# Kernel optimization log

Measured on AMD Instinct MI355X. Metric: run time of the kernel, lower is better.

Reference implementation:

```python
import jax, jax.numpy as jnp
import numpy as np

IMG_C = 256
GC = 32  # graph_channel; must equal graph feature dim 32 for the residual


def setup_inputs() -> dict:
    key = jax.random.key(0)
    ks = jax.random.split(key, 10)
    B, N, WH_SIDE = 8, 4096, 64
    s = lambda fan_in: 1.0 / np.sqrt(fan_in)
    return {
        "input_graph": jax.random.normal(ks[0], (B, N, GC), jnp.float32),
        "input_image": jax.random.normal(ks[1], (B, IMG_C, WH_SIDE, WH_SIDE), jnp.float32),
        # Conv1d(kernel=1) weights stored as [out, in]
        "Wq": jax.random.uniform(ks[2], (GC, 32), jnp.float32, -s(32), s(32)),
        "bq": jax.random.uniform(ks[3], (GC,), jnp.float32, -s(32), s(32)),
        "Wk": jax.random.uniform(ks[4], (GC, IMG_C), jnp.float32, -s(IMG_C), s(IMG_C)),
        "bk": jax.random.uniform(ks[5], (GC,), jnp.float32, -s(IMG_C), s(IMG_C)),
        "Wv": jax.random.uniform(ks[6], (GC, IMG_C), jnp.float32, -s(IMG_C), s(IMG_C)),
        "bv": jax.random.uniform(ks[7], (GC,), jnp.float32, -s(IMG_C), s(IMG_C)),
        "Wc": jax.random.uniform(ks[8], (GC, GC), jnp.float32, -s(GC), s(GC)),
        "bc": jax.random.uniform(ks[9], (GC,), jnp.float32, -s(GC), s(GC)),
    }


def reference(input_graph, input_image, Wq, bq, Wk, bk, Wv, bv, Wc, bc):
    B, C, W, H = input_image.shape
    img = input_image.reshape(B, C, W * H)                      # [B, C, L]
    # 1x1 conv projections == channel matmuls
    K = jnp.einsum('oc,bcl->bol', Wk, img) + bk[None, :, None]  # [B, GC, L]
    V = jnp.einsum('oc,bcl->bol', Wv, img) + bv[None, :, None]  # [B, GC, L]
    # Q: graph [B, N, 32] -> conv over channel dim -> [B, N, GC]
    Q = jnp.einsum('oc,bnc->bno', Wq, input_graph) + bq[None, None, :]
    att = jnp.einsum('bno,bol->bnl', Q, K) / jnp.sqrt(jnp.float32(GC))  # [B, N, L]
    # NOTE: original softmax is over dim=1 (the node/query axis)
    att = jax.nn.softmax(att, axis=1)
    message = jnp.einsum('bol,bnl->bon', V, att)                # [B, GC, N]
    out = input_graph.transpose(0, 2, 1) + (
        jnp.einsum('oc,bcn->bon', Wc, message) + bc[None, :, None]
    )                                                           # [B, GC, N]
    return out.transpose(0, 2, 1)                               # [B, N, GC]
```

## Files before the change

### kernel.cpp

```cpp
#include <hip/hip_runtime.h>

#define BB 8
#define NN 4096
#define LL 4096
#define CC 256

typedef short bf16x8 __attribute__((ext_vector_type(8)));
typedef _Float16 f16x8 __attribute__((ext_vector_type(8)));
typedef __fp16 hf16x2 __attribute__((ext_vector_type(2)));
typedef float f32x4 __attribute__((ext_vector_type(4)));

__device__ __forceinline__ short f2bf(float f) {
  union { float f; unsigned u; } v; v.f = f;
  unsigned r = v.u + 0x7fffu + ((v.u >> 16) & 1u);
  return (short)(r >> 16);
}
__device__ __forceinline__ bf16x8 ld8(const float* __restrict__ fp) {
  float4 a = *(const float4*)fp;
  float4 b = *(const float4*)(fp + 4);
  bf16x8 r;
  r[0] = f2bf(a.x); r[1] = f2bf(a.y); r[2] = f2bf(a.z); r[3] = f2bf(a.w);
  r[4] = f2bf(b.x); r[5] = f2bf(b.y); r[6] = f2bf(b.z); r[7] = f2bf(b.w);
  return r;
}

__global__ __launch_bounds__(256) void ka_proj(
    const float* __restrict__ graph, const float* __restrict__ img,
    const float* __restrict__ Wq, const float* __restrict__ bq,
    const float* __restrict__ Wk, const float* __restrict__ bk,
    const float* __restrict__ Wv, const float* __restrict__ bv,
    short* __restrict__ Qb, short* __restrict__ Kt, _Float16* __restrict__ Vt,
    float* __restrict__ Zbuf)
{
  const int tid = threadIdx.x;
  const int w = tid >> 6, lane = tid & 63, lo = lane & 15, q = lane >> 4;
  const int bid = blockIdx.x;
  if (bid < 512) {
    const int b = bid >> 6;
    if (tid < 64) Zbuf[(size_t)b * LL + ((bid & 63) << 6) + tid] = 0.0f;
    const int lt = ((bid & 63) << 6) + (w << 4);
    f32x4 aK0 = {0,0,0,0}, aK1 = {0,0,0,0}, aV0 = {0,0,0,0}, aV1 = {0,0,0,0};
    const float* ib = img + (size_t)b * CC * LL + lt + lo;
    #pragma unroll
    for (int cs = 0; cs < 8; ++cs) {
      const int c0 = cs * 32 + q * 8;
      bf16x8 bi;
      #pragma unroll
      for (int j = 0; j < 8; ++j) bi[j] = f2bf(ib[(size_t)(c0 + j) * LL]);
      bf16x8 wk0 = ld8(Wk + lo * CC + c0);
      bf16x8 wk1 = ld8(Wk + (lo + 16) * CC + c0);
      bf16x8 wv0 = ld8(Wv + lo * CC + c0);
      bf16x8 wv1 = ld8(Wv + (lo + 16) * CC + c0);
      aK0 = __builtin_amdgcn_mfma_f32_16x16x32_bf16(wk0, bi, aK0, 0, 0, 0);
      aK1 = __builtin_amdgcn_mfma_f32_16x16x32_bf16(wk1, bi, aK1, 0, 0, 0);
      aV0 = __builtin_amdgcn_mfma_f32_16x16x32_bf16(wv0, bi, aV0, 0, 0, 0);
      aV1 = __builtin_amdgcn_mfma_f32_16x16x32_bf16(wv1, bi, aV1, 0, 0, 0);
    }
    const float kscale = 0.2550348663f;
    const size_t row = ((size_t)b * LL + lt + lo) * 32;
    short4 s0, s1;
    s0.x = f2bf((aK0[0] + bk[q * 4 + 0]) * kscale);
    s0.y = f2bf((aK0[1] + bk[q * 4 + 1]) * kscale);
    s0.z = f2bf((aK0[2] + bk[q * 4 + 2]) * kscale);
    s0.w = f2bf((aK0[3] + bk[q * 4 + 3]) * kscale);
    s1.x = f2bf((aK1[0] + bk[16 + q * 4 + 0]) * kscale);
    s1.y = f2bf((aK1[1] + bk[16 + q * 4 + 1]) * kscale);
    s1.z = f2bf((aK1[2] + bk[16 + q * 4 + 2]) * kscale);
    s1.w = f2bf((aK1[3] + bk[16 + q * 4 + 3]) * kscale);
    *(short4*)(Kt + row + q * 4) = s0;
    *(short4*)(Kt + row + 16 + q * 4) = s1;
    union { hf16x2 h[2]; uint2 u; } p0, p1;
    p0.h[0] = __builtin_amdgcn_cvt_pkrtz(aV0[0] + bv[q * 4 + 0], aV0[1] + bv[q * 4 + 1]);
    p0.h[1] = __builtin_amdgcn_cvt_pkrtz(aV0[2] + bv[q * 4 + 2], aV0[3] + bv[q * 4 + 3]);
    p1.h[0] = __builtin_amdgcn_cvt_pkrtz(aV1[0] + bv[16 + q * 4 + 0], aV1[1] + bv[16 + q * 4 + 1]);
    p1.h[1] = __builtin_amdgcn_cvt_pkrtz(aV1[2] + bv[16 + q * 4 + 2], aV1[3] + bv[16 + q * 4 + 3]);
    *(uint2*)(Vt + row + q * 4) = p0.u;
    *(uint2*)(Vt + row + 16 + q * 4) = p1.u;
  } else {
    const int t = bid - 512;
    const int b = t >> 6;
    const int nt = ((t & 63) << 6) + (w << 4);
    bf16x8 ag = ld8(graph + ((size_t)b * NN + nt + lo) * 32 + q * 8);
    bf16x8 w0 = ld8(Wq + lo * 32 + q * 8);
    bf16x8 w1 = ld8(Wq + (lo + 16) * 32 + q * 8);
    f32x4 z = {0,0,0,0};
    f32x4 a0 = __builtin_amdgcn_mfma_f32_16x16x32_bf16(ag, w0, z, 0, 0, 0);
    f32x4 a1 = __builtin_amdgcn_mfma_f32_16x16x32_bf16(ag, w1, z, 0, 0, 0);
    const float b0 = bq[lo], b1 = bq[lo + 16];
    #pragma unroll
    for (int r = 0; r < 4; ++r) {
      const size_t rowq = ((size_t)b * NN + nt + q * 4 + r) * 32;
      Qb[rowq + lo] = f2bf(a0[r] + b0);
      Qb[rowq + 16 + lo] = f2bf(a1[r] + b1);
    }
  }
}

__global__ __launch_bounds__(256) void kb1_z(
    const short* __restrict__ Qb, const short* __restrict__ Kt,
    float* __restrict__ Z)
{
  const int tid = threadIdx.x;
  const int w = tid >> 6, lane = tid & 63, lo = lane & 15, q = lane >> 4;
  const int bid = blockIdx.x;
  const int b = bid & 7;
  const int t = bid >> 3;
  const int l0 = (t >> 2) << 7;
  const int nq = t & 3;
  bf16x8 kf[8];
  #pragma unroll
  for (int f = 0; f < 8; ++f)
    kf[f] = *(const bf16x8*)(Kt + ((size_t)b * LL + l0 + f * 16 + lo) * 32 + q * 8);
  float za[8][4] = {{0}};
  const short* qbase = Qb + ((size_t)b * NN + nq * 1024 + w * 256 + lo) * 32 + q * 8;
  #pragma unroll 4
  for (int it = 0; it < 16; ++it) {
    bf16x8 qf = *(const bf16x8*)(qbase + it * 512);
    #pragma unroll
    for (int f = 0; f < 8; ++f) {
      f32x4 z = {0,0,0,0};
      f32x4 c = __builtin_amdgcn_mfma_f32_16x16x32_bf16(kf[f], qf, z, 0, 0, 0);
      #pragma unroll
      for (int r = 0; r < 4; ++r) za[f][r] += __builtin_amdgcn_exp2f(c[r]);
    }
  }
  #pragma unroll
  for (int m = 1; m < 16; m <<= 1)
    #pragma unroll
    for (int f = 0; f < 8; ++f)
      #pragma unroll
      for (int r = 0; r < 4; ++r)
        za[f][r] += __shfl_xor(za[f][r], m, 64);
  if (lo == 0) {
    #pragma unroll
    for (int f = 0; f < 8; ++f)
      #pragma unroll
      for (int r = 0; r < 4; ++r)
        atomicAdd(&Z[(size_t)b * LL + l0 + f * 16 + q * 4 + r], za[f][r]);
  }
}

__global__ __launch_bounds__(256) void kb2_scale(
    const _Float16* __restrict__ Vt, const float* __restrict__ Z,
    _Float16* __restrict__ Vpp)
{
  const int tid = threadIdx.x;
  const int b = blockIdx.x >> 6;
  const int l = ((blockIdx.x & 63) << 6) + (tid & 63);
  const int og = tid >> 6;
  const float inv = __builtin_amdgcn_rcpf(Z[(size_t)b * LL + l]) * 4096.0f;
  const f16x8 vv = *(const f16x8*)(Vt + ((size_t)b * LL + l) * 32 + og * 8);
  #pragma unroll
  for (int j = 0; j < 8; ++j)
    Vpp[((size_t)b * 32 + og * 8 + j) * LL + l] = (_Float16)((float)vv[j] * inv);
}

__global__ __launch_bounds__(256) void kc_attn(
    const short* __restrict__ Qb, const short* __restrict__ Kt,
    const _Float16* __restrict__ Vpp, const float* __restrict__ graph,
    const float* __restrict__ Wc, const float* __restrict__ bc,
    float* __restrict__ out)
{
  __shared__ __align__(16) unsigned char smem[4 * 9216];
  const int tid = threadIdx.x;
  const int w = tid >> 6, lane = tid & 63, lo = lane & 15, q = lane >> 4;
  const int b = blockIdx.x & 7;
  const int n0 = ((int)blockIdx.x >> 3) << 6;
  _Float16* Pw = (_Float16*)(smem + w * 9216);
  bf16x8 qf[4];
  #pragma unroll
  for (int nq = 0; nq < 4; ++nq)
    qf[nq] = *(const bf16x8*)(Qb + ((size_t)b * NN + n0 + nq * 16 + lo) * 32 + q * 8);
  f32x4 m[4][2];
  #pragma unroll
  for (int nq = 0; nq < 4; ++nq) {
    m[nq][0] = (f32x4){0,0,0,0};
    m[nq][1] = (f32x4){0,0,0,0};
  }
  const short* ktb = Kt + (size_t)b * LL * 32 + lo * 32 + q * 8;
  const _Float16* vb0 = Vpp + ((size_t)b * 32 + lo) * LL;
  const _Float16* vb1 = vb0 + (size_t)16 * LL;
  const int lc0 = w * 16;
  for (int lc = lc0; lc < lc0 + 16; ++lc) {
    const int lbase = lc * 64;
    bf16x8 kf[4];
    #pragma unroll
    for (int f = 0; f < 4; ++f)
      kf[f] = *(const bf16x8*)(ktb + (size_t)(lbase + f * 16) * 32);
    f16x8 vA0 = *(const f16x8*)(vb0 + lbase + q * 8);
    f16x8 vA1 = *(const f16x8*)(vb0 + lbase + 32 + q * 8);
    f16x8 vB0 = *(const f16x8*)(vb1 + lbase + q * 8);
    f16x8 vB1 = *(const f16x8*)(vb1 + lbase + 32 + q * 8);
    #pragma unroll
    for (int nq = 0; nq < 4; ++nq)
      #pragma unroll
      for (int f = 0; f < 4; ++f) {
        f32x4 z = {0,0,0,0};
        f32x4 c = __builtin_amdgcn_mfma_f32_16x16x32_bf16(kf[f], qf[nq], z, 0, 0, 0);
        union { hf16x2 h[2]; uint2 u; } pk;
        pk.h[0] = __builtin_amdgcn_cvt_pkrtz(__builtin_amdgcn_exp2f(c[0]),
                                             __builtin_amdgcn_exp2f(c[1]));
        pk.h[1] = __builtin_amdgcn_cvt_pkrtz(__builtin_amdgcn_exp2f(c[2]),
                                             __builtin_amdgcn_exp2f(c[3]));
        *(uint2*)&Pw[(nq * 16 + lo) * 72 + f * 16 + q * 4] = pk.u;
      }
    #pragma unroll
    for (int nq = 0; nq < 4; ++nq) {
      f16x8 pa0 = *(const f16x8*)&Pw[(nq * 16 + lo) * 72 + q * 8];
      f16x8 pa1 = *(const f16x8*)&Pw[(nq * 16 + lo) * 72 + 32 + q * 8];
      m[nq][0] = __builtin_amdgcn_mfma_f32_16x16x32_f16(pa0, vA0, m[nq][0], 0, 0, 0);
      m[nq][1] = __builtin_amdgcn_mfma_f32_16x16x32_f16(pa0, vB0, m[nq][1], 0, 0, 0);
      m[nq][0] = __builtin_amdgcn_mfma_f32_16x16x32_f16(pa1, vA1, m[nq][0], 0, 0, 0);
      m[nq][1] = __builtin_amdgcn_mfma_f32_16x16x32_f16(pa1, vB1, m[nq][1], 0, 0, 0);
    }
  }
  float* MSw = (float*)(smem + w * 9216);
  #pragma unroll
  for (int nq = 0; nq < 4; ++nq)
    #pragma unroll
    for (int r = 0; r < 4; ++r) {
      MSw[(nq * 16 + q * 4 + r) * 36 + lo] = m[nq][0][r];
      MSw[(nq * 16 + q * 4 + r) * 36 + 16 + lo] = m[nq][1][r];
    }
  __syncthreads();
  const float* MS = (const float*)smem;
  const int o = lane & 31, nh = lane >> 5;
  float wcr[32];
  #pragma unroll
  for (int c4 = 0; c4 < 8; ++c4) {
    float4 wc4 = *(const float4*)(Wc + o * 32 + c4 * 4);
    wcr[c4 * 4 + 0] = wc4.x * (1.0f / 4096.0f);
    wcr[c4 * 4 + 1] = wc4.y * (1.0f / 4096.0f);
    wcr[c4 * 4 + 2] = wc4.z * (1.0f / 4096.0f);
    wcr[c4 * 4 + 3] = wc4.w * (1.0f / 4096.0f);
  }
  const float bcv = bc[o];
  #pragma unroll
  for (int rr = 0; rr < 8; ++rr) {
    const int nl = w * 16 + nh * 8 + rr;
    f32x4 s = {0,0,0,0};
    #pragma unroll
    for (int cc = 0; cc < 8; ++cc) {
      f32x4 ma = *(const f32x4*)&MS[0 * 2304 + nl * 36 + cc * 4];
      f32x4 mb = *(const f32x4*)&MS[1 * 2304 + nl * 36 + cc * 4];
      f32x4 mc = *(const f32x4*)&MS[2 * 2304 + nl * 36 + cc * 4];
      f32x4 md = *(const f32x4*)&MS[3 * 2304 + nl * 36 + cc * 4];
      f32x4 m4 = ma + mb + mc + md;
      s[0] += wcr[cc * 4 + 0] * m4[0];
      s[1] += wcr[cc * 4 + 1] * m4[1];
      s[2] += wcr[cc * 4 + 2] * m4[2];
      s[3] += wcr[cc * 4 + 3] * m4[3];
    }
    const size_t idx = ((size_t)b * NN + n0 + nl) * 32 + o;
    out[idx] = s[0] + s[1] + s[2] + s[3] + bcv + graph[idx];
  }
}

extern "C" void kernel_launch(void* const* d_in, const int* in_sizes, int n_in,
                              void* d_out, int out_size, void* d_ws, size_t ws_size,
                              hipStream_t stream) {
  const float* graph = (const float*)d_in[0];
  const float* img   = (const float*)d_in[1];
  const float* Wq    = (const float*)d_in[2];
  const float* bq    = (const float*)d_in[3];
  const float* Wk    = (const float*)d_in[4];
  const float* bk    = (const float*)d_in[5];
  const float* Wv    = (const float*)d_in[6];
  const float* bv    = (const float*)d_in[7];
  const float* Wc    = (const float*)d_in[8];
  const float* bc    = (const float*)d_in[9];
  char* ws = (char*)d_ws;
  short*    Qb  = (short*)(ws + 0);
  short*    Kt  = (short*)(ws + 2097152);
  _Float16* Vt  = (_Float16*)(ws + 4194304);
  _Float16* Vpp = (_Float16*)(ws + 6291456);
  float*    Zb  = (float*)(ws + 8388608);
  ka_proj<<<dim3(1024), dim3(256), 0, stream>>>(graph, img, Wq, bq, Wk, bk, Wv, bv,
                                                Qb, Kt, Vt, Zb);
  kb1_z<<<dim3(1024), dim3(256), 0, stream>>>(Qb, Kt, Zb);
  kb2_scale<<<dim3(512), dim3(256), 0, stream>>>(Vt, Zb, Vpp);
  kc_attn<<<dim3(512), dim3(256), 0, stream>>>(Qb, Kt, Vpp, graph, Wc, bc,
                                               (float*)d_out);
}
```

Before: 175.9 us.

## Double node tile per block in attention kernel, split L across eight waves

The attention kernel now handles 128 query nodes per block with 512 threads, so there are 8 waves instead of 4, each covering 8 L-chunks instead of 16. Each K/V fragment loaded from memory is reused across twice as many query rows, which cuts global K/V traffic per output. The per-wave P buffer shrinks and the partial-sum reduction runs in four phases over smem, each bracketed by barriers. The cost is more accumulator registers (8x2 f32x4), half as many blocks (256), extra syncs, and an 8-way rather than 4-way smem reduction.

```diff
diff --git a/kernel.cpp b/kernel.cpp
--- a/kernel.cpp
+++ b/kernel.cpp
@@ -155,33 +155,33 @@
     Vpp[((size_t)b * 32 + og * 8 + j) * LL + l] = (_Float16)((float)vv[j] * inv);
 }
 
-__global__ __launch_bounds__(256) void kc_attn(
+__global__ __launch_bounds__(512) void kc_attn(
     const short* __restrict__ Qb, const short* __restrict__ Kt,
     const _Float16* __restrict__ Vpp, const float* __restrict__ graph,
     const float* __restrict__ Wc, const float* __restrict__ bc,
     float* __restrict__ out)
 {
-  __shared__ __align__(16) unsigned char smem[4 * 9216];
+  __shared__ __align__(16) unsigned char smem[8 * 4608];
   const int tid = threadIdx.x;
   const int w = tid >> 6, lane = tid & 63, lo = lane & 15, q = lane >> 4;
   const int b = blockIdx.x & 7;
-  const int n0 = ((int)blockIdx.x >> 3) << 6;
-  _Float16* Pw = (_Float16*)(smem + w * 9216);
-  bf16x8 qf[4];
-  #pragma unroll
-  for (int nq = 0; nq < 4; ++nq)
+  const int n0 = ((int)blockIdx.x >> 3) << 7;
+  _Float16* Pw = (_Float16*)(smem + w * 4608);
+  bf16x8 qf[8];
+  #pragma unroll
+  for (int nq = 0; nq < 8; ++nq)
     qf[nq] = *(const bf16x8*)(Qb + ((size_t)b * NN + n0 + nq * 16 + lo) * 32 + q * 8);
-  f32x4 m[4][2];
-  #pragma unroll
-  for (int nq = 0; nq < 4; ++nq) {
+  f32x4 m[8][2];
+  #pragma unroll
+  for (int nq = 0; nq < 8; ++nq) {
     m[nq][0] = (f32x4){0,0,0,0};
     m[nq][1] = (f32x4){0,0,0,0};
   }
   const short* ktb = Kt + (size_t)b * LL * 32 + lo * 32 + q * 8;
   const _Float16* vb0 = Vpp + ((size_t)b * 32 + lo) * LL;
   const _Float16* vb1 = vb0 + (size_t)16 * LL;
-  const int lc0 = w * 16;
-  for (int lc = lc0; lc < lc0 + 16; ++lc) {
+  const int lc0 = w * 8;
+  for (int lc = lc0; lc < lc0 + 8; ++lc) {
     const int lbase = lc * 64;
     bf16x8 kf[4];
     #pragma unroll
@@ -192,38 +192,34 @@
     f16x8 vB0 = *(const f16x8*)(vb1 + lbase + q * 8);
     f16x8 vB1 = *(const f16x8*)(vb1 + lbase + 32 + q * 8);
     #pragma unroll
-    for (int nq = 0; nq < 4; ++nq)
-      #pragma unroll
-      for (int f = 0; f < 4; ++f) {
-        f32x4 z = {0,0,0,0};
-        f32x4 c = __builtin_amdgcn_mfma_f32_16x16x32_bf16(kf[f], qf[nq], z, 0, 0, 0);
-        union { hf16x2 h[2]; uint2 u; } pk;
-        pk.h[0] = __builtin_amdgcn_cvt_pkrtz(__builtin_amdgcn_exp2f(c[0]),
-                                             __builtin_amdgcn_exp2f(c[1]));
-        pk.h[1] = __builtin_amdgcn_cvt_pkrtz(__builtin_amdgcn_exp2f(c[2]),
-                                             __builtin_amdgcn_exp2f(c[3]));
-        *(uint2*)&Pw[(nq * 16 + lo) * 72 + f * 16 + q * 4] = pk.u;
-      }
-    #pragma unroll
-    for (int nq = 0; nq < 4; ++nq) {
-      f16x8 pa0 = *(const f16x8*)&Pw[(nq * 16 + lo) * 72 + q * 8];
-      f16x8 pa1 = *(const f16x8*)&Pw[(nq * 16 + lo) * 72 + 32 + q * 8];
-      m[nq][0] = __builtin_amdgcn_mfma_f32_16x16x32_f16(pa0, vA0, m[nq][0], 0, 0, 0);
-      m[nq][1] = __builtin_amdgcn_mfma_f32_16x16x32_f16(pa0, vB0, m[nq][1], 0, 0, 0);
-      m[nq][0] = __builtin_amdgcn_mfma_f32_16x16x32_f16(pa1, vA1, m[nq][0], 0, 0, 0);
-      m[nq][1] = __builtin_amdgcn_mfma_f32_16x16x32_f16(pa1, vB1, m[nq][1], 0, 0, 0);
-    }
-  }
-  float* MSw = (float*)(smem + w * 9216);
-  #pragma unroll
-  for (int nq = 0; nq < 4; ++nq)
-    #pragma unroll
-    for (int r = 0; r < 4; ++r) {
-      MSw[(nq * 16 + q * 4 + r) * 36 + lo] = m[nq][0][r];
-      MSw[(nq * 16 + q * 4 + r) * 36 + 16 + lo] = m[nq][1][r];
-    }
-  __syncthreads();
-  const float* MS = (const float*)smem;
+    for (int p = 0; p < 4; ++p) {
+      #pragma unroll
+      for (int h = 0; h < 2; ++h) {
+        const int nq = p * 2 + h;
+        #pragma unroll
+        for (int f = 0; f < 4; ++f) {
+          f32x4 z = {0,0,0,0};
+          f32x4 c = __builtin_amdgcn_mfma_f32_16x16x32_bf16(kf[f], qf[nq], z, 0, 0, 0);
+          union { hf16x2 hh[2]; uint2 u; } pk;
+          pk.hh[0] = __builtin_amdgcn_cvt_pkrtz(__builtin_amdgcn_exp2f(c[0]),
+                                                __builtin_amdgcn_exp2f(c[1]));
+          pk.hh[1] = __builtin_amdgcn_cvt_pkrtz(__builtin_amdgcn_exp2f(c[2]),
+                                                __builtin_amdgcn_exp2f(c[3]));
+          *(uint2*)&Pw[(h * 16 + lo) * 72 + f * 16 + q * 4] = pk.u;
+        }
+      }
+      #pragma unroll
+      for (int h = 0; h < 2; ++h) {
+        const int nq = p * 2 + h;
+        f16x8 pa0 = *(const f16x8*)&Pw[(h * 16 + lo) * 72 + q * 8];
+        f16x8 pa1 = *(const f16x8*)&Pw[(h * 16 + lo) * 72 + 32 + q * 8];
+        m[nq][0] = __builtin_amdgcn_mfma_f32_16x16x32_f16(pa0, vA0, m[nq][0], 0, 0, 0);
+        m[nq][1] = __builtin_amdgcn_mfma_f32_16x16x32_f16(pa0, vB0, m[nq][1], 0, 0, 0);
+        m[nq][0] = __builtin_amdgcn_mfma_f32_16x16x32_f16(pa1, vA1, m[nq][0], 0, 0, 0);
+        m[nq][1] = __builtin_amdgcn_mfma_f32_16x16x32_f16(pa1, vB1, m[nq][1], 0, 0, 0);
+      }
+    }
+  }
   const int o = lane & 31, nh = lane >> 5;
   float wcr[32];
   #pragma unroll
@@ -235,24 +231,39 @@
     wcr[c4 * 4 + 3] = wc4.w * (1.0f / 4096.0f);
   }
   const float bcv = bc[o];
-  #pragma unroll
-  for (int rr = 0; rr < 8; ++rr) {
-    const int nl = w * 16 + nh * 8 + rr;
-    f32x4 s = {0,0,0,0};
-    #pragma unroll
-    for (int cc = 0; cc < 8; ++cc) {
-      f32x4 ma = *(const f32x4*)&MS[0 * 2304 + nl * 36 + cc * 4];
-      f32x4 mb = *(const f32x4*)&MS[1 * 2304 + nl * 36 + cc * 4];
-      f32x4 mc = *(const f32x4*)&MS[2 * 2304 + nl * 36 + cc * 4];
-      f32x4 md = *(const f32x4*)&MS[3 * 2304 + nl * 36 + cc * 4];
-      f32x4 m4 = ma + mb + mc + md;
-      s[0] += wcr[cc * 4 + 0] * m4[0];
-      s[1] += wcr[cc * 4 + 1] * m4[1];
-      s[2] += wcr[cc * 4 + 2] * m4[2];
-      s[3] += wcr[cc * 4 + 3] * m4[3];
-    }
-    const size_t idx = ((size_t)b * NN + n0 + nl) * 32 + o;
-    out[idx] = s[0] + s[1] + s[2] + s[3] + bcv + graph[idx];
+  float* MSw = (float*)(smem + w * 4608);
+  const float* MS = (const float*)smem;
+  #pragma unroll
+  for (int p = 0; p < 4; ++p) {
+    __syncthreads();
+    #pragma unroll
+    for (int h = 0; h < 2; ++h) {
+      const int nq = p * 2 + h;
+      #pragma unroll
+      for (int r = 0; r < 4; ++r) {
+        MSw[(h * 16 + q * 4 + r) * 36 + lo] = m[nq][0][r];
+        MSw[(h * 16 + q * 4 + r) * 36 + 16 + lo] = m[nq][1][r];
+      }
+    }
+    __syncthreads();
+    #pragma unroll
+    for (int rr = 0; rr < 2; ++rr) {
+      const int nr = w * 4 + nh * 2 + rr;
+      f32x4 s = {0,0,0,0};
+      #pragma unroll
+      for (int cc = 0; cc < 8; ++cc) {
+        f32x4 a4 = *(const f32x4*)&MS[0 * 1152 + nr * 36 + cc * 4];
+        #pragma unroll
+        for (int k = 1; k < 8; ++k)
+          a4 += *(const f32x4*)&MS[k * 1152 + nr * 36 + cc * 4];
+        s[0] += wcr[cc * 4 + 0] * a4[0];
+        s[1] += wcr[cc * 4 + 1] * a4[1];
+        s[2] += wcr[cc * 4 + 2] * a4[2];
+        s[3] += wcr[cc * 4 + 3] * a4[3];
+      }
+      const size_t idx = ((size_t)b * NN + n0 + p * 32 + nr) * 32 + o;
+      out[idx] = s[0] + s[1] + s[2] + s[3] + bcv + graph[idx];
+    }
   }
 }
 
@@ -279,6 +290,6 @@
                                                 Qb, Kt, Vt, Zb);
   kb1_z<<<dim3(1024), dim3(256), 0, stream>>>(Qb, Kt, Zb);
   kb2_scale<<<dim3(512), dim3(256), 0, stream>>>(Vt, Zb, Vpp);
-  kc_attn<<<dim3(512), dim3(256), 0, stream>>>(Qb, Kt, Vpp, graph, Wc, bc,
+  kc_attn<<<dim3(256), dim3(512), 0, stream>>>(Qb, Kt, Vpp, graph, Wc, bc,
                                                (float*)d_out);
 }
```

Result: no change. 176.2 us, median of 2 (+0.2%).
